# Kernel tuning notes

Measured on AMD Instinct MI355X. Metric: run time of the kernel, lower is better.

The kernel has to match this reference:

```python
import jax, jax.numpy as jnp
import numpy as np

N_NODES = 50000
N_EDGES = 800000
F_IN = 11
HID = 128
N_ACT = 6


def _gcn_conv(x, W, b, src, dst, n):
    # PyG GCNConv: x' = D^{-1/2}(A+I)D^{-1/2} (x W) + b, with self-loops.
    h = x @ W  # [N, H]
    ones = jnp.ones(src.shape[0], dtype=h.dtype)
    deg = jax.ops.segment_sum(ones, dst, num_segments=n) + 1.0  # +1 self-loop
    dinv = jax.lax.rsqrt(deg)
    enorm = dinv[src] * dinv[dst]  # [E]
    msg = h[src] * enorm[:, None]  # gather + scale
    agg = jax.ops.segment_sum(msg, dst, num_segments=n)
    agg = agg + h * (dinv * dinv)[:, None]  # self-loop contribution (norm = 1/deg)
    return agg + b


def _mlp2(x, W1, b1, W2, b2):
    return jax.nn.relu(x @ W1 + b1) @ W2 + b2


def setup_inputs() -> dict:
    key = jax.random.key(0)
    ks = jax.random.split(key, 16)
    def g(k, shape, scale):
        return jax.random.normal(k, shape, dtype=jnp.float32) * scale
    x = g(ks[0], (N_NODES, F_IN), 1.0)
    edge_index = jax.random.randint(ks[1], (2, N_EDGES), 0, N_NODES, dtype=jnp.int64)
    return {
        "x": x,
        "edge_index": edge_index,
        "W1": g(ks[2], (F_IN, HID), 1.0 / np.sqrt(F_IN)),
        "b1": jnp.zeros((HID,), jnp.float32),
        "W2": g(ks[3], (HID, HID), 1.0 / np.sqrt(HID)),
        "b2": jnp.zeros((HID,), jnp.float32),
        "W3": g(ks[4], (HID, HID), 1.0 / np.sqrt(HID)),
        "b3": jnp.zeros((HID,), jnp.float32),
        "Wv1": g(ks[5], (HID, HID), 1.0 / np.sqrt(HID)),
        "bv1": jnp.zeros((HID,), jnp.float32),
        "Wv2": g(ks[6], (HID, 1), 1.0 / np.sqrt(HID)),
        "bv2": jnp.zeros((1,), jnp.float32),
        "Wa1": g(ks[7], (HID, HID), 1.0 / np.sqrt(HID)),
        "ba1": jnp.zeros((HID,), jnp.float32),
        "Wa2": g(ks[8], (HID, N_ACT), 1.0 / np.sqrt(HID)),
        "ba2": jnp.zeros((N_ACT,), jnp.float32),
    }


def reference(x, edge_index, W1, b1, W2, b2, W3, b3,
              Wv1, bv1, Wv2, bv2, Wa1, ba1, Wa2, ba2):
    src, dst = edge_index[0], edge_index[1]
    n = x.shape[0]
    h = jax.nn.relu(_gcn_conv(x, W1, b1, src, dst, n))
    h = jax.nn.relu(_gcn_conv(h, W2, b2, src, dst, n))
    h = jax.nn.relu(_gcn_conv(h, W3, b3, src, dst, n))
    # global_mean_pool with batch = zeros -> single-graph mean over nodes
    g = jnp.mean(h, axis=0, keepdims=True)  # [1, HID]
    value = _mlp2(g, Wv1, bv1, Wv2, bv2)          # [1, 1]
    advantage = _mlp2(g, Wa1, ba1, Wa2, ba2)      # [1, N_ACT]
    q = value + (advantage - jnp.mean(advantage, axis=-1, keepdims=True))
    return q
```

## Files before the change

### kernel.cpp

```cpp
#include <hip/hip_runtime.h>

#define HID 128
#define F_IN 11
#define FP 16
#define N_ACT 6
#define EPB 2048
#define LMAX 6144
#define CAP 8192

typedef __bf16 bf16;
typedef __bf16 v8bf __attribute__((ext_vector_type(8)));
typedef float f32x4 __attribute__((ext_vector_type(4)));
typedef float v2f __attribute__((ext_vector_type(2)));

__device__ inline float lo16(unsigned u) { return __uint_as_float(u << 16); }
__device__ inline float hi16(unsigned u) { return __uint_as_float(u & 0xffff0000u); }
__device__ inline unsigned pk2(float a, float b) {
  union { bf16 h; unsigned short u; } x, y;
  x.h = (bf16)a; y.h = (bf16)b;
  return ((unsigned)y.u << 16) | x.u;
}
__device__ inline v2f fp8_dec_lo(unsigned v) {
  return __builtin_amdgcn_cvt_pk_f32_fp8(v, false);
}
__device__ inline v2f fp8_dec_hi(unsigned v) {
  return __builtin_amdgcn_cvt_pk_f32_fp8(v, true);
}
__device__ inline unsigned fp8_enc2_lo(float a, float b, unsigned old) {
  return __builtin_amdgcn_cvt_pk_fp8_f32(a, b, old, false);
}
__device__ inline unsigned fp8_enc2_hi(float a, float b, unsigned old) {
  return __builtin_amdgcn_cvt_pk_fp8_f32(a, b, old, true);
}
__device__ inline unsigned char fp8_enc1(float v) {
  return (unsigned char)(__builtin_amdgcn_cvt_pk_fp8_f32(v, v, 0u, false) & 0xffu);
}


__global__ __launch_bounds__(256) void k_init(int* __restrict__ gcur,
                                              float* __restrict__ gsum,
                                              unsigned* __restrict__ xsN,
                                              unsigned* __restrict__ H8aN,
                                              unsigned* __restrict__ H8bN, int nbkt) {
  int t = threadIdx.x;
  if (t < nbkt) gcur[t] = t * CAP;
  if (t < HID) gsum[t] = 0.f;
  if (t < 8) xsN[t] = 0u;
  if (t < 32) { H8aN[t] = 0u; H8bN[t] = 0u; }
}


__global__ __launch_bounds__(256) void k_part(const int* __restrict__ esrc,
                                              const int* __restrict__ edst,
                                              int* __restrict__ gcur,
                                              unsigned* __restrict__ ebuf,
                                              const float* __restrict__ W2,
                                              const float* __restrict__ W3,
                                              bf16* __restrict__ WT2,
                                              bf16* __restrict__ WT3,
                                              int E, int nbkt) {
  __shared__ int hist[256], lofs[256], lcur[256], gbase[256];
  __shared__ unsigned sbuf[EPB];
  int t = threadIdx.x;
  hist[t] = 0;
  if (blockIdx.x < 64) {
    int i = blockIdx.x * 256 + t;
    int nn = i >> 7, k = i & 127;
    WT2[i] = (bf16)W2[k * 128 + nn];
    WT3[i] = (bf16)W3[k * 128 + nn];
  }
  __syncthreads();
  int start = blockIdx.x * EPB, end = min(E, start + EPB);
  unsigned u[8];
#pragma unroll
  for (int i = 0; i < 8; ++i) {
    int e = start + t + i * 256;
    if (e < end) {
      int s = esrc[e], d = edst[e];
      u[i] = ((unsigned)d << 16) | (unsigned)s;
      atomicAdd(&hist[d >> 8], 1);
    }
  }
  __syncthreads();
  int h = hist[t];
  lofs[t] = h;
  __syncthreads();
  for (int off = 1; off < 256; off <<= 1) {
    int x = (t >= off) ? lofs[t - off] : 0;
    __syncthreads();
    lofs[t] += x;
    __syncthreads();
  }
  lcur[t] = lofs[t] - h;
  if (t < nbkt && h) gbase[t] = atomicAdd(&gcur[t], h);
  __syncthreads();
#pragma unroll
  for (int i = 0; i < 8; ++i) {
    int e = start + t + i * 256;
    if (e < end) {
      int b = (int)(u[i] >> 24);
      int p = atomicAdd(&lcur[b], 1);
      sbuf[p] = u[i];
    }
  }
  __syncthreads();
  int m = end - start;
  for (int i = t; i < m; i += 256) {
    unsigned v = sbuf[i];
    int b = (int)(v >> 24);
    int excl = lofs[b] - hist[b];
    ebuf[gbase[b] + (i - excl)] = v;
  }
}

__global__ __launch_bounds__(1024) void k_local(const unsigned* __restrict__ ebuf,
                                                const int* __restrict__ gcur,
                                                int2* __restrict__ rbe,
                                                float* __restrict__ dinv,
                                                unsigned short* __restrict__ cs,
                                                const float* __restrict__ x,
                                                bf16* __restrict__ xs, int n) {
  __shared__ int hist[256], lofs[256], cur[256], realh[256];
  __shared__ float dsh[256];
  __shared__ unsigned sb[LMAX];
  int b = blockIdx.x, t = threadIdx.x;
  int rb = b * CAP, re = gcur[b];
  int m = re - rb;
  int nbase = b << 8;
  bool fit = (m <= LMAX);
  if (t < 256) hist[t] = 0;
  __syncthreads();
  if (fit) {
    for (int i = t; i < m; i += 1024) {
      unsigned u = ebuf[rb + i];
      sb[i] = u;
      atomicAdd(&hist[(int)(u >> 16) - nbase], 1);
    }
  } else {
    for (int i = t; i < m; i += 1024)
      atomicAdd(&hist[(int)(ebuf[rb + i] >> 16) - nbase], 1);
  }
  __syncthreads();
  int h = 0, hp = 0;
  if (t < 256) {
    h = hist[t];
    realh[t] = h;
    hp = (h + 15) & ~15;
    lofs[t] = hp;
  }
  __syncthreads();
  for (int off = 1; off < 256; off <<= 1) {
    int v = (t < 256 && t >= off) ? lofs[t - off] : 0;
    __syncthreads();
    if (t < 256) lofs[t] += v;
    __syncthreads();
  }
  if (t < 256) {
    int pexcl = lofs[t] - hp;
    cur[t] = rb + pexcl;
    float dv = rsqrtf((float)h + 1.0f);
    dsh[t] = dv;
    int g = nbase + t;
    if (g < n) {
      rbe[g] = make_int2(rb + pexcl, rb + pexcl + hp);
      dinv[g] = dv;
    }
  }
  __syncthreads();
  if (fit) {
    for (int i = t; i < m; i += 1024) {
      unsigned u = sb[i];
      int p = atomicAdd(&cur[(int)(u >> 16) - nbase], 1);
      cs[p] = (unsigned short)(u & 0xffffu);
    }
  } else {
    for (int i = t; i < m; i += 1024) {
      unsigned u = ebuf[rb + i];
      int p = atomicAdd(&cur[(int)(u >> 16) - nbase], 1);
      cs[p] = (unsigned short)(u & 0xffffu);
    }
  }
  __syncthreads();
  if (t < 256) {
    int hh = realh[t];
    int hpp = (hh + 15) & ~15;
    int base = cur[t];
    for (int i = hh; i < hpp; ++i) cs[base + (i - hh)] = (unsigned short)n;
  }
  for (int i = t; i < 256 * FP; i += 1024) {
    int node = nbase + (i >> 4), c = i & 15;
    if (node < n)
      xs[(size_t)node * FP + c] =
          (bf16)((c < F_IN) ? x[(size_t)node * F_IN + c] * dsh[i >> 4] : 0.f);
  }
}


__global__ __launch_bounds__(256) void k_layer1(const bf16* __restrict__ xs,
                                                const float* __restrict__ dinv,
                                                const int2* __restrict__ rbe,
                                                const unsigned short* __restrict__ cs,
                                                const float* __restrict__ W1,
                                                const float* __restrict__ b1,
                                                unsigned* __restrict__ H8, int n) {
  __shared__ float Ws[F_IN * HID];
  __shared__ float A1s[64][17];
  int tid = threadIdx.x;
  int n0 = blockIdx.x * 64;
  for (int i = tid; i < F_IN * HID; i += 256) Ws[i] = W1[i];
  int wave = tid >> 6, lane = tid & 63;
  int g8 = lane >> 3, c = lane & 7;
  const unsigned* xs2 = (const unsigned*)xs;
#pragma unroll
  for (int r = 0; r < 2; ++r) {
    int row = wave * 16 + r * 8 + g8;
    int node = n0 + row;
    unsigned sv = 0;
    int j = 0, jend = 0;
    float dd = 0.f;
    if (node < n) {
      sv = xs2[(size_t)node * 8 + c];
      int2 be = rbe[node];
      j = be.x; jend = be.y;
      dd = dinv[node];
    }
    float ax = lo16(sv), ay = hi16(sv);
    for (; j < jend; j += 4) {
#pragma unroll
      for (int k = 0; k < 4; ++k) {
        unsigned v = xs2[(size_t)cs[j + k] * 8 + c];
        ax += lo16(v);
        ay += hi16(v);
      }
    }
    A1s[row][c * 2] = ax * dd;
    A1s[row][c * 2 + 1] = ay * dd;
  }
  __syncthreads();
  int tc = tid & 15, tr = tid >> 4;
  float bb[8];
#pragma unroll
  for (int j = 0; j < 8; ++j) bb[j] = b1[tc * 8 + j];
#pragma unroll
  for (int i = 0; i < 4; ++i) {
    int row = tr * 4 + i;
    int node = n0 + row;
    if (node >= n) continue;
    float acc[8];
#pragma unroll
    for (int j = 0; j < 8; ++j) acc[j] = 0.f;
#pragma unroll
    for (int k = 0; k < F_IN; ++k) {
      float xk = A1s[row][k];
      const float* wr = &Ws[k * HID + tc * 8];
#pragma unroll
      for (int j = 0; j < 8; ++j) acc[j] = fmaf(xk, wr[j], acc[j]);
    }
    float dd = dinv[node];
    float o[8];
#pragma unroll
    for (int j = 0; j < 8; ++j) o[j] = fmaxf(acc[j] + bb[j], 0.f) * dd;
    unsigned w0 = 0, w1 = 0;
    w0 = fp8_enc2_lo(o[0], o[1], w0);
    w0 = fp8_enc2_hi(o[2], o[3], w0);
    w1 = fp8_enc2_lo(o[4], o[5], w1);
    w1 = fp8_enc2_hi(o[6], o[7], w1);
    ((uint2*)H8)[(size_t)node * 16 + tc] = make_uint2(w0, w1);
  }
}


template <bool FINAL>
__global__ __launch_bounds__(512) void k_layer(const unsigned* __restrict__ tab,
                                               const float* __restrict__ dinv,
                                               const int2* __restrict__ rbe,
                                               const unsigned short* __restrict__ cs,
                                               const bf16* __restrict__ WT,
                                               const float* __restrict__ b,
                                               unsigned char* __restrict__ H8,
                                               float* __restrict__ gsum, int n) {
  __shared__ bf16 Asm[32 * 128];
  __shared__ float colacc[128];
  int tid = threadIdx.x;
  int n0 = blockIdx.x * 32;
  if (FINAL && tid < 128) colacc[tid] = 0.f;
  int wave = tid >> 6, lane = tid & 63;
  int sub = lane >> 5;
  int c = lane & 31;
#pragma unroll
  for (int r = 0; r < 2; ++r) {
    int row = wave * 4 + r * 2 + sub;
    int node = n0 + row;
    v2f acc01 = (v2f){0.f, 0.f}, acc23 = (v2f){0.f, 0.f};
    float dd = 0.f;
    int j = 0, jend = 0;
    if (node < n) {
      unsigned sv = tab[(size_t)node * 32 + c];
      acc01 = fp8_dec_lo(sv);
      acc23 = fp8_dec_hi(sv);
      int2 be = rbe[node];
      j = be.x; jend = be.y;
      dd = dinv[node];
    }
    for (; j < jend; j += 16) {
      uint4 cv0 = *(const uint4*)(cs + j);
      uint4 cv1 = *(const uint4*)(cs + j + 8);
      unsigned sx[16];
      sx[0] = cv0.x & 0xffffu;  sx[1] = cv0.x >> 16;
      sx[2] = cv0.y & 0xffffu;  sx[3] = cv0.y >> 16;
      sx[4] = cv0.z & 0xffffu;  sx[5] = cv0.z >> 16;
      sx[6] = cv0.w & 0xffffu;  sx[7] = cv0.w >> 16;
      sx[8] = cv1.x & 0xffffu;  sx[9] = cv1.x >> 16;
      sx[10] = cv1.y & 0xffffu; sx[11] = cv1.y >> 16;
      sx[12] = cv1.z & 0xffffu; sx[13] = cv1.z >> 16;
      sx[14] = cv1.w & 0xffffu; sx[15] = cv1.w >> 16;
      unsigned vv[16];
#pragma unroll
      for (int k = 0; k < 16; ++k) vv[k] = tab[(size_t)sx[k] * 32 + c];
#pragma unroll
      for (int k = 0; k < 16; ++k) {
        acc01 += fp8_dec_lo(vv[k]);
        acc23 += fp8_dec_hi(vv[k]);
      }
    }
    int kc = c >> 1, half = c & 1;
    uint2 w = make_uint2(pk2(acc01.x * dd, acc01.y * dd),
                         pk2(acc23.x * dd, acc23.y * dd));
    *(uint2*)((char*)Asm + row * 256 + ((kc ^ (row & 7)) << 4) + (half << 3)) = w;
  }
  __syncthreads();
  int l15 = lane & 15, g = lane >> 4;
  int rg = (wave & 1) * 16;
  int cbase = (wave >> 1) * 32;
  f32x4 acc[2];
#pragma unroll
  for (int f = 0; f < 2; ++f) acc[f] = (f32x4){0.f, 0.f, 0.f, 0.f};
  int arow = rg + l15;
#pragma unroll
  for (int kk = 0; kk < 4; ++kk) {
    int kc = kk * 4 + g;
    v8bf a = *(const v8bf*)((const char*)Asm + arow * 256 + ((kc ^ (arow & 7)) << 4));
#pragma unroll
    for (int f = 0; f < 2; ++f) {
      int nrow = cbase + f * 16 + l15;
      v8bf bfr = *(const v8bf*)(WT + (size_t)nrow * 128 + kc * 8);
      acc[f] = __builtin_amdgcn_mfma_f32_16x16x32_bf16(a, bfr, acc[f], 0, 0, 0);
    }
  }
  int nodebase = n0 + rg + g * 4;
  if (FINAL) {
#pragma unroll
    for (int f = 0; f < 2; ++f) {
      int col = cbase + f * 16 + l15;
      float bias = b[col];
      float sf = 0.f;
#pragma unroll
      for (int j = 0; j < 4; ++j) {
        int node = nodebase + j;
        if (node < n) sf += fmaxf(acc[f][j] + bias, 0.f);
      }
      atomicAdd(&colacc[col], sf);
    }
    __syncthreads();
    if (tid < 128) atomicAdd(&gsum[tid], colacc[tid]);
  } else {
    float dv[4];
#pragma unroll
    for (int j = 0; j < 4; ++j)
      dv[j] = (nodebase + j < n) ? dinv[nodebase + j] : 1.f;
#pragma unroll
    for (int f = 0; f < 2; ++f) {
      int col = cbase + f * 16 + l15;
      float bias = b[col];
#pragma unroll
      for (int j = 0; j < 4; ++j) {
        int node = nodebase + j;
        if (node < n) {
          float v = fmaxf(acc[f][j] + bias, 0.f) * dv[j];
          H8[(size_t)node * 128 + col] = fp8_enc1(v);
        }
      }
    }
  }
}


__global__ __launch_bounds__(128) void k_head(const float* __restrict__ gsum,
    const float* __restrict__ Wv1, const float* __restrict__ bv1,
    const float* __restrict__ Wv2, const float* __restrict__ bv2,
    const float* __restrict__ Wa1, const float* __restrict__ ba1,
    const float* __restrict__ Wa2, const float* __restrict__ ba2,
    float* __restrict__ out, int n) {
  __shared__ float gs[HID], ha[HID], red[2], advs[N_ACT], vsh;
  int t = threadIdx.x;
  gs[t] = gsum[t] * (1.0f / (float)n);
  __syncthreads();
  float av = bv1[t], aa = ba1[t];
  for (int k = 0; k < HID; ++k) {
    float gk = gs[k];
    av = fmaf(gk, Wv1[k * HID + t], av);
    aa = fmaf(gk, Wa1[k * HID + t], aa);
  }
  float hv = fmaxf(av, 0.f);
  ha[t] = fmaxf(aa, 0.f);
  float pv = hv * Wv2[t];
#pragma unroll
  for (int o = 32; o > 0; o >>= 1) pv += __shfl_down(pv, o);
  if ((t & 63) == 0) red[t >> 6] = pv;
  __syncthreads();
  if (t == 0) vsh = red[0] + red[1] + bv2[0];
  if (t < N_ACT) {
    float adv = ba2[t];
    for (int j = 0; j < HID; ++j) adv = fmaf(ha[j], Wa2[j * N_ACT + t], adv);
    advs[t] = adv;
  }
  __syncthreads();
  if (t < N_ACT) {
    float m = 0.f;
#pragma unroll
    for (int a = 0; a < N_ACT; ++a) m += advs[a];
    m *= (1.0f / N_ACT);
    out[t] = vsh + advs[t] - m;
  }
}


extern "C" void kernel_launch(void* const* d_in, const int* in_sizes, int n_in,
                              void* d_out, int out_size, void* d_ws, size_t ws_size,
                              hipStream_t stream) {
  const float* x   = (const float*)d_in[0];
  const int*   ei  = (const int*)d_in[1];
  const float* W1  = (const float*)d_in[2];
  const float* b1  = (const float*)d_in[3];
  const float* W2  = (const float*)d_in[4];
  const float* b2  = (const float*)d_in[5];
  const float* W3  = (const float*)d_in[6];
  const float* b3  = (const float*)d_in[7];
  const float* Wv1 = (const float*)d_in[8];
  const float* bv1 = (const float*)d_in[9];
  const float* Wv2 = (const float*)d_in[10];
  const float* bv2 = (const float*)d_in[11];
  const float* Wa1 = (const float*)d_in[12];
  const float* ba1 = (const float*)d_in[13];
  const float* Wa2 = (const float*)d_in[14];
  const float* ba2 = (const float*)d_in[15];
  float* out = (float*)d_out;

  const int N = in_sizes[0] / F_IN;
  const int E = in_sizes[1] / 2;
  const int* esrc = ei;
  const int* edst = ei + E;
  const int nbkt = (N + 255) >> 8;
  const int gE = (E + EPB - 1) / EPB;

  char* p = (char*)d_ws;
  auto alloc = [&](size_t bytes) {
    void* r = (void*)p;
    p += (bytes + 1023) & ~(size_t)1023;
    return r;
  };
  unsigned* ebuf   = (unsigned*)alloc((size_t)nbkt * CAP * 4);
  int*   gcur      = (int*)alloc((size_t)nbkt * 4);
  int2*  rbe       = (int2*)alloc((size_t)N * 8);
  float* dinv      = (float*)alloc((size_t)N * 4);
  unsigned short* cs = (unsigned short*)alloc((size_t)nbkt * CAP * 2);
  bf16*  xs        = (bf16*)alloc((size_t)(N + 1) * FP * 2);
  bf16*  WT2       = (bf16*)alloc(128 * 128 * 2);
  bf16*  WT3       = (bf16*)alloc(128 * 128 * 2);
  unsigned* H8a    = (unsigned*)alloc((size_t)(N + 1) * 128);
  unsigned* H8b    = (unsigned*)alloc((size_t)(N + 1) * 128);
  float* gsum      = (float*)alloc(HID * 4);

  k_init<<<1, 256, 0, stream>>>(gcur, gsum, (unsigned*)(xs + (size_t)N * FP),
                                H8a + (size_t)N * 32, H8b + (size_t)N * 32, nbkt);
  k_part<<<gE, 256, 0, stream>>>(esrc, edst, gcur, ebuf, W2, W3, WT2, WT3, E, nbkt);
  k_local<<<nbkt, 1024, 0, stream>>>(ebuf, gcur, rbe, dinv, cs, x, xs, N);

  k_layer1<<<(N + 63) / 64, 256, 0, stream>>>(xs, dinv, rbe, cs, W1, b1, H8a, N);

  int gL = (N + 31) / 32;
  k_layer<false><<<gL, 512, 0, stream>>>(H8a, dinv, rbe, cs, WT2, b2,
                                         (unsigned char*)H8b, gsum, N);
  k_layer<true><<<gL, 512, 0, stream>>>(H8b, dinv, rbe, cs, WT3, b3,
                                        (unsigned char*)nullptr, gsum, N);

  k_head<<<1, 128, 0, stream>>>(gsum, Wv1, bv1, Wv2, bv2, Wa1, ba1, Wa2, ba2, out, N);
}
```

Measured before the change: 145.9 us.

## Software-pipeline neighbor gathers and double node tile per block in GCN layer

The layer kernel now handles 64 nodes per block instead of 32. Each wave aggregates four rows and runs an MFMA tile of 16 rows by 64 columns, so each wave loads more weight fragments per A fragment. The gather loop is software-pipelined: the next 16 neighbor rows are loaded before the previous batch is decoded, which hides gather latency. The cost is more live registers, which may reduce occupancy, plus a doubled shared A tile and half as many blocks.

```diff
diff --git a/kernel.cpp b/kernel.cpp
--- a/kernel.cpp
+++ b/kernel.cpp
@@ -270,6 +270,27 @@
 }
 
 
+
+#define LOAD8(p, cv)                                      \
+  p##0 = tab[(size_t)(cv.x & 0xffffu) * 32 + c];          \
+  p##1 = tab[(size_t)(cv.x >> 16) * 32 + c];              \
+  p##2 = tab[(size_t)(cv.y & 0xffffu) * 32 + c];          \
+  p##3 = tab[(size_t)(cv.y >> 16) * 32 + c];              \
+  p##4 = tab[(size_t)(cv.z & 0xffffu) * 32 + c];          \
+  p##5 = tab[(size_t)(cv.z >> 16) * 32 + c];              \
+  p##6 = tab[(size_t)(cv.w & 0xffffu) * 32 + c];          \
+  p##7 = tab[(size_t)(cv.w >> 16) * 32 + c];
+
+#define CONSUME8(p)                                       \
+  acc01 += fp8_dec_lo(p##0); acc23 += fp8_dec_hi(p##0);   \
+  acc01 += fp8_dec_lo(p##1); acc23 += fp8_dec_hi(p##1);   \
+  acc01 += fp8_dec_lo(p##2); acc23 += fp8_dec_hi(p##2);   \
+  acc01 += fp8_dec_lo(p##3); acc23 += fp8_dec_hi(p##3);   \
+  acc01 += fp8_dec_lo(p##4); acc23 += fp8_dec_hi(p##4);   \
+  acc01 += fp8_dec_lo(p##5); acc23 += fp8_dec_hi(p##5);   \
+  acc01 += fp8_dec_lo(p##6); acc23 += fp8_dec_hi(p##6);   \
+  acc01 += fp8_dec_lo(p##7); acc23 += fp8_dec_hi(p##7);
+
 template <bool FINAL>
 __global__ __launch_bounds__(512) void k_layer(const unsigned* __restrict__ tab,
                                                const float* __restrict__ dinv,
@@ -279,17 +300,17 @@
                                                const float* __restrict__ b,
                                                unsigned char* __restrict__ H8,
                                                float* __restrict__ gsum, int n) {
-  __shared__ bf16 Asm[32 * 128];
+  __shared__ bf16 Asm[64 * 128];
   __shared__ float colacc[128];
   int tid = threadIdx.x;
-  int n0 = blockIdx.x * 32;
+  int n0 = blockIdx.x * 64;
   if (FINAL && tid < 128) colacc[tid] = 0.f;
   int wave = tid >> 6, lane = tid & 63;
   int sub = lane >> 5;
   int c = lane & 31;
 #pragma unroll
-  for (int r = 0; r < 2; ++r) {
-    int row = wave * 4 + r * 2 + sub;
+  for (int r = 0; r < 4; ++r) {
+    int row = wave * 8 + r * 2 + sub;
     int node = n0 + row;
     v2f acc01 = (v2f){0.f, 0.f}, acc23 = (v2f){0.f, 0.f};
     float dd = 0.f;
@@ -302,26 +323,24 @@
       j = be.x; jend = be.y;
       dd = dinv[node];
     }
-    for (; j < jend; j += 16) {
+    if (j < jend) {
+      unsigned a0, a1, a2, a3, a4, a5, a6, a7;
+      unsigned b0, b1, b2, b3, b4, b5, b6, b7;
       uint4 cv0 = *(const uint4*)(cs + j);
       uint4 cv1 = *(const uint4*)(cs + j + 8);
-      unsigned sx[16];
-      sx[0] = cv0.x & 0xffffu;  sx[1] = cv0.x >> 16;
-      sx[2] = cv0.y & 0xffffu;  sx[3] = cv0.y >> 16;
-      sx[4] = cv0.z & 0xffffu;  sx[5] = cv0.z >> 16;
-      sx[6] = cv0.w & 0xffffu;  sx[7] = cv0.w >> 16;
-      sx[8] = cv1.x & 0xffffu;  sx[9] = cv1.x >> 16;
-      sx[10] = cv1.y & 0xffffu; sx[11] = cv1.y >> 16;
-      sx[12] = cv1.z & 0xffffu; sx[13] = cv1.z >> 16;
-      sx[14] = cv1.w & 0xffffu; sx[15] = cv1.w >> 16;
-      unsigned vv[16];
-#pragma unroll
-      for (int k = 0; k < 16; ++k) vv[k] = tab[(size_t)sx[k] * 32 + c];
-#pragma unroll
-      for (int k = 0; k < 16; ++k) {
-        acc01 += fp8_dec_lo(vv[k]);
-        acc23 += fp8_dec_hi(vv[k]);
+      LOAD8(a, cv0)
+      LOAD8(b, cv1)
+      j += 16;
+      for (; j < jend; j += 16) {
+        uint4 nv0 = *(const uint4*)(cs + j);
+        CONSUME8(a)
+        LOAD8(a, nv0)
+        uint4 nv1 = *(const uint4*)(cs + j + 8);
+        CONSUME8(b)
+        LOAD8(b, nv1)
       }
+      CONSUME8(a)
+      CONSUME8(b)
     }
     int kc = c >> 1, half = c & 1;
     uint2 w = make_uint2(pk2(acc01.x * dd, acc01.y * dd),
@@ -330,19 +349,19 @@
   }
   __syncthreads();
   int l15 = lane & 15, g = lane >> 4;
-  int rg = (wave & 1) * 16;
-  int cbase = (wave >> 1) * 32;
-  f32x4 acc[2];
-#pragma unroll
-  for (int f = 0; f < 2; ++f) acc[f] = (f32x4){0.f, 0.f, 0.f, 0.f};
+  int rg = (wave & 3) * 16;
+  int cg = (wave >> 2) * 64;
+  f32x4 acc[4];
+#pragma unroll
+  for (int f = 0; f < 4; ++f) acc[f] = (f32x4){0.f, 0.f, 0.f, 0.f};
   int arow = rg + l15;
 #pragma unroll
   for (int kk = 0; kk < 4; ++kk) {
     int kc = kk * 4 + g;
     v8bf a = *(const v8bf*)((const char*)Asm + arow * 256 + ((kc ^ (arow & 7)) << 4));
 #pragma unroll
-    for (int f = 0; f < 2; ++f) {
-      int nrow = cbase + f * 16 + l15;
+    for (int f = 0; f < 4; ++f) {
+      int nrow = cg + f * 16 + l15;
       v8bf bfr = *(const v8bf*)(WT + (size_t)nrow * 128 + kc * 8);
       acc[f] = __builtin_amdgcn_mfma_f32_16x16x32_bf16(a, bfr, acc[f], 0, 0, 0);
     }
@@ -350,8 +369,8 @@
   int nodebase = n0 + rg + g * 4;
   if (FINAL) {
 #pragma unroll
-    for (int f = 0; f < 2; ++f) {
-      int col = cbase + f * 16 + l15;
+    for (int f = 0; f < 4; ++f) {
+      int col = cg + f * 16 + l15;
       float bias = b[col];
       float sf = 0.f;
 #pragma unroll
@@ -369,8 +388,8 @@
     for (int j = 0; j < 4; ++j)
       dv[j] = (nodebase + j < n) ? dinv[nodebase + j] : 1.f;
 #pragma unroll
-    for (int f = 0; f < 2; ++f) {
-      int col = cbase + f * 16 + l15;
+    for (int f = 0; f < 4; ++f) {
+      int col = cg + f * 16 + l15;
       float bias = b[col];
 #pragma unroll
       for (int j = 0; j < 4; ++j) {
@@ -383,6 +402,9 @@
     }
   }
 }
+
+#undef LOAD8
+#undef CONSUME8
 
 
 __global__ __launch_bounds__(128) void k_head(const float* __restrict__ gsum,
@@ -478,7 +500,7 @@
 
   k_layer1<<<(N + 63) / 64, 256, 0, stream>>>(xs, dinv, rbe, cs, W1, b1, H8a, N);
 
-  int gL = (N + 31) / 32;
+  int gL = (N + 63) / 64;
   k_layer<false><<<gL, 512, 0, stream>>>(H8a, dinv, rbe, cs, WT2, b2,
                                          (unsigned char*)H8b, gsum, N);
   k_layer<true><<<gL, 512, 0, stream>>>(H8b, dinv, rbe, cs, WT3, b3,
```

Measured after the change: 147.5 us. Within noise of the previous version (+1.1%).
